# Optimization experiments

Measured on AMD Instinct MI355X. Metric: run time of the kernel, lower is better.

## Reference

```python
import jax, jax.numpy as jnp
import numpy as np

N_NODES = 50000
N_EDGES = 800000
D = 128
N_GRAPHS = 128
N_CLASSES = 10
BN_EPS = 1e-5


def setup_inputs() -> dict:
    key = jax.random.key(0)
    ks = jax.random.split(key, 8)
    x = jax.random.normal(ks[0], (N_NODES, D), dtype=jnp.float32)
    edge_index = jax.random.randint(ks[1], (2, N_EDGES), 0, N_NODES, dtype=jnp.int64)
    batch = jnp.sort(jax.random.randint(ks[2], (N_NODES,), 0, N_GRAPHS, dtype=jnp.int64))
    s = 1.0 / np.sqrt(D)
    W1a = jax.random.normal(ks[3], (D, D), dtype=jnp.float32) * s
    W1b = jax.random.normal(ks[4], (D, D), dtype=jnp.float32) * s
    W2a = jax.random.normal(ks[5], (D, D), dtype=jnp.float32) * s
    W2b = jax.random.normal(ks[6], (D, D), dtype=jnp.float32) * s
    Wo = jax.random.normal(ks[7], (D, N_CLASSES), dtype=jnp.float32) * s
    z = jnp.zeros((D,), jnp.float32)
    o = jnp.ones((D,), jnp.float32)
    return dict(x=x, edge_index=edge_index, batch=batch,
                W1a=W1a, b1a=z, W1b=W1b, b1b=z, g1=o, be1=z,
                W2a=W2a, b2a=z, W2b=W2b, b2b=z, g2=o, be2=z,
                Wo=Wo, bo=jnp.zeros((N_CLASSES,), jnp.float32))


def _gin_conv(x, edge_index, Wa, ba, Wb, bb):
    # message passing: gather source features, scatter-add to targets (eps=0)
    msgs = x[edge_index[0]]                                   # [E, D]
    agg = jax.ops.segment_sum(msgs, edge_index[1], num_segments=x.shape[0])
    h = agg + x                                               # (1+eps)*x + sum_j x_j
    h = jnp.maximum(h @ Wa + ba, 0.0)                         # Linear -> ReLU
    return h @ Wb + bb                                        # Linear


def _bn_relu(h, gamma, beta):
    # BatchNorm1d (training mode: batch stats, biased var) + ReLU
    mu = jnp.mean(h, axis=0)
    var = jnp.mean(jnp.square(h - mu), axis=0)
    hn = (h - mu) * jax.lax.rsqrt(var + BN_EPS) * gamma + beta
    return jnp.maximum(hn, 0.0)


def reference(x, edge_index, batch,
              W1a, b1a, W1b, b1b, g1, be1,
              W2a, b2a, W2b, b2b, g2, be2,
              Wo, bo):
    h = _gin_conv(x, edge_index, W1a, b1a, W1b, b1b)
    h = _bn_relu(h, g1, be1)
    h = _gin_conv(h, edge_index, W2a, b2a, W2b, b2b)
    h = _bn_relu(h, g2, be2)
    pooled = jax.ops.segment_sum(h, batch, num_segments=N_GRAPHS)  # global_add_pool
    return pooled @ Wo + bo
```

## Files before the change

### kernel.cpp

```cpp
#include <hip/hip_runtime.h>

typedef __attribute__((ext_vector_type(8))) short bf16x8;
typedef __attribute__((ext_vector_type(4))) float f32x4;
typedef __attribute__((ext_vector_type(2))) float f32x2;
typedef __attribute__((ext_vector_type(2))) unsigned u32x2;

#define N_NODES 50000
#define N_EDGES 800000
#define DIM 128
#define N_GRAPHS 128
#define N_CLASSES 10
#define BN_EPS 1e-5f
#define FBLK ((N_NODES + 63) / 64)
#define NPART (FBLK * 4)
#define RED_NB 64
#define RED_ROWS ((NPART + RED_NB - 1) / RED_NB)

#define NBUCK 196
#define FILL_NB 400
#define FILL_PER (N_EDGES / FILL_NB)
#define BMAX 6144

static __device__ __forceinline__ unsigned short f2bf(float f) {
    unsigned u = __float_as_uint(f);
    u += 0x7FFF + ((u >> 16) & 1);
    return (unsigned short)(u >> 16);
}
static __device__ __forceinline__ float bf_lo(unsigned u) { return __uint_as_float(u << 16); }
static __device__ __forceinline__ float bf_hi(unsigned u) { return __uint_as_float(u & 0xffff0000u); }
static __device__ __forceinline__ unsigned packbf(float a, float b) {
    return (unsigned)f2bf(a) | ((unsigned)f2bf(b) << 16);
}

__global__ __launch_bounds__(256) void cvt_x(const f32x2* __restrict__ x,
                                             unsigned* __restrict__ xb, int n) {
    int t = blockIdx.x * 256 + threadIdx.x;
    if (t < n) { f32x2 v = x[t]; xb[t] = packbf(v[0], v[1]); }
}

__global__ __launch_bounds__(256) void bucket_count(const int* __restrict__ ei,
                                                    int* __restrict__ gbcnt) {
    __shared__ int cnt[NBUCK];
    int tid = threadIdx.x;
    if (tid < NBUCK) cnt[tid] = 0;
    __syncthreads();
    int e0 = blockIdx.x * FILL_PER;
    for (int c = tid; c < FILL_PER; c += 256) {
        int dst = ei[N_EDGES + e0 + c];
        atomicAdd(&cnt[dst >> 8], 1);
    }
    __syncthreads();
    if (tid < NBUCK) atomicAdd(&gbcnt[tid], cnt[tid]);
}

__global__ __launch_bounds__(256) void bucket_scan(const int* __restrict__ gbcnt,
                                                   int* __restrict__ boff,
                                                   int* __restrict__ gcur) {
    __shared__ int buf[256];
    int t = threadIdx.x;
    int v = (t < NBUCK) ? gbcnt[t] : 0;
    buf[t] = v;
    __syncthreads();
#pragma unroll
    for (int off = 1; off < 256; off <<= 1) {
        int u = (t >= off) ? buf[t - off] : 0;
        __syncthreads();
        buf[t] += u;
        __syncthreads();
    }
    if (t < NBUCK) { int ex = buf[t] - v; boff[t] = ex; gcur[t] = ex; }
    if (t == 0) boff[NBUCK] = N_EDGES;
}

__global__ __launch_bounds__(256) void bucket_fill(const int* __restrict__ ei,
                                                   int* __restrict__ gcur,
                                                   unsigned* __restrict__ gbuf) {
    __shared__ unsigned ent[FILL_PER];
    __shared__ unsigned srt[FILL_PER];
    __shared__ int cnt[256], c2[256], lofs[256], gbase[256];
    int tid = threadIdx.x;
    int e0 = blockIdx.x * FILL_PER;
    cnt[tid] = 0; c2[tid] = 0;
    __syncthreads();
    for (int i = tid; i < FILL_PER; i += 256) {
        int src = ei[e0 + i];
        int dst = ei[N_EDGES + e0 + i];
        ent[i] = (unsigned)src | ((unsigned)(dst & 255) << 16) | ((unsigned)(dst >> 8) << 24);
        atomicAdd(&cnt[dst >> 8], 1);
    }
    __syncthreads();
    int v = cnt[tid];
    lofs[tid] = v;
    __syncthreads();
#pragma unroll
    for (int off = 1; off < 256; off <<= 1) {
        int u = (tid >= off) ? lofs[tid - off] : 0;
        __syncthreads();
        lofs[tid] += u;
        __syncthreads();
    }
    int excl = lofs[tid] - v;
    lofs[tid] = excl;
    if (tid < NBUCK && v > 0) gbase[tid] = atomicAdd(&gcur[tid], v);
    __syncthreads();
    for (int i = tid; i < FILL_PER; i += 256) {
        unsigned w = ent[i];
        int b = w >> 24;
        int r = atomicAdd(&c2[b], 1);
        srt[lofs[b] + r] = w;
    }
    __syncthreads();
    for (int i = tid; i < FILL_PER; i += 256) {
        unsigned w = srt[i];
        int b = w >> 24;
        gbuf[gbase[b] + (i - lofs[b])] = w;
    }
}

__global__ __launch_bounds__(256) void csr_build(const unsigned* __restrict__ gbuf,
                                                 const int* __restrict__ boff,
                                                 unsigned short* __restrict__ csr16,
                                                 int* __restrict__ row_start) {
    __shared__ unsigned ent[BMAX];
    __shared__ unsigned short csl[BMAX];
    __shared__ int cnt[256], c2[256], offs[256];
    int b = blockIdx.x, t = threadIdx.x;
    int base = boff[b], n = boff[b + 1] - base;
    for (int i = t; i < n; i += 256) ent[i] = gbuf[base + i];
    cnt[t] = 0; c2[t] = 0;
    __syncthreads();
    for (int i = t; i < n; i += 256) atomicAdd(&cnt[(ent[i] >> 16) & 255], 1);
    __syncthreads();
    int v = cnt[t];
    offs[t] = v;
    __syncthreads();
#pragma unroll
    for (int off = 1; off < 256; off <<= 1) {
        int u = (t >= off) ? offs[t - off] : 0;
        __syncthreads();
        offs[t] += u;
        __syncthreads();
    }
    int excl = offs[t] - v;
    int node = b * 256 + t;
    if (node < N_NODES) row_start[node] = base + excl;
    if (b == NBUCK - 1 && t == 0) row_start[N_NODES] = N_EDGES;
    __syncthreads();
    offs[t] = excl;
    __syncthreads();
    for (int i = t; i < n; i += 256) {
        unsigned w = ent[i];
        int d = (w >> 16) & 255;
        int r = atomicAdd(&c2[d], 1);
        csl[offs[d] + r] = (unsigned short)(w & 0xffffu);
    }
    __syncthreads();
    for (int i = t; i < n; i += 256) csr16[base + i] = csl[i];
}

__global__ __launch_bounds__(256) void graph_starts(const int* __restrict__ batch,
                                                    int* __restrict__ gs) {
    int g = blockIdx.x * 256 + threadIdx.x;
    if (g > N_GRAPHS) return;
    int lo = 0, hi = N_NODES;
    while (lo < hi) {
        int mid = (lo + hi) >> 1;
        if (batch[mid] < g) lo = mid + 1; else hi = mid;
    }
    gs[g] = lo;
}

template <bool BN>
__global__ __launch_bounds__(256) void aggregate_bf(const unsigned* __restrict__ F,
                                                    unsigned* __restrict__ out,
                                                    const int* __restrict__ row_start,
                                                    const unsigned short* __restrict__ csr16,
                                                    const float* __restrict__ scale,
                                                    const float* __restrict__ shift) {
    int wave = threadIdx.x >> 6, lane = threadIdx.x & 63;
    int v = blockIdx.x * 4 + wave;
    if (v >= N_NODES) return;
    float sc0 = 0.f, sc1 = 0.f, sh0 = 0.f, sh1 = 0.f;
    if (BN) {
        f32x2 s2 = ((const f32x2*)scale)[lane];
        f32x2 h2 = ((const f32x2*)shift)[lane];
        sc0 = s2[0]; sc1 = s2[1]; sh0 = h2[0]; sh1 = h2[1];
    }
    unsigned u = F[(size_t)v * 64 + lane];
    float a0 = bf_lo(u), a1 = bf_hi(u);
    if (BN) { a0 = fmaxf(a0 * sc0 + sh0, 0.f); a1 = fmaxf(a1 * sc1 + sh1, 0.f); }
    int e = row_start[v], end = row_start[v + 1];
    for (; e + 3 < end; e += 4) {
        unsigned ua = F[(size_t)csr16[e] * 64 + lane];
        unsigned ub = F[(size_t)csr16[e + 1] * 64 + lane];
        unsigned uc = F[(size_t)csr16[e + 2] * 64 + lane];
        unsigned ud = F[(size_t)csr16[e + 3] * 64 + lane];
        float p0 = bf_lo(ua), p1 = bf_hi(ua), q0 = bf_lo(ub), q1 = bf_hi(ub);
        float r0 = bf_lo(uc), r1 = bf_hi(uc), s0 = bf_lo(ud), s1 = bf_hi(ud);
        if (BN) {
            p0 = fmaxf(p0 * sc0 + sh0, 0.f); p1 = fmaxf(p1 * sc1 + sh1, 0.f);
            q0 = fmaxf(q0 * sc0 + sh0, 0.f); q1 = fmaxf(q1 * sc1 + sh1, 0.f);
            r0 = fmaxf(r0 * sc0 + sh0, 0.f); r1 = fmaxf(r1 * sc1 + sh1, 0.f);
            s0 = fmaxf(s0 * sc0 + sh0, 0.f); s1 = fmaxf(s1 * sc1 + sh1, 0.f);
        }
        a0 += (p0 + q0) + (r0 + s0);
        a1 += (p1 + q1) + (r1 + s1);
    }
    for (; e < end; ++e) {
        unsigned ua = F[(size_t)csr16[e] * 64 + lane];
        float p0 = bf_lo(ua), p1 = bf_hi(ua);
        if (BN) { p0 = fmaxf(p0 * sc0 + sh0, 0.f); p1 = fmaxf(p1 * sc1 + sh1, 0.f); }
        a0 += p0; a1 += p1;
    }
    out[(size_t)v * 64 + lane] = packbf(a0, a1);
}

__global__ __launch_bounds__(256) void prep_w(const float* __restrict__ W0,
                                              const float* __restrict__ W1,
                                              const float* __restrict__ W2,
                                              const float* __restrict__ W3,
                                              unsigned short* __restrict__ wf) {
    int t = blockIdx.x * 256 + threadIdx.x;
    if (t >= 4 * 16384) return;
    int m = t >> 14, rem = t & 16383;
    int e = rem & 7, lane = (rem >> 3) & 63, fi = rem >> 9;
    int ks = fi & 3, n = fi >> 2;
    int col = n * 16 + (lane & 15);
    int k = ks * 32 + ((lane >> 4) << 3) + e;
    const float* W = (m == 0) ? W0 : (m == 1) ? W1 : (m == 2) ? W2 : W3;
    wf[t] = f2bf(W[k * DIM + col]);
}

__global__ __launch_bounds__(256, 3) void fused_layer(
        const unsigned short* __restrict__ A,
        const bf16x8* __restrict__ wfA_g,
        const bf16x8* __restrict__ wfB_g,
        const float* __restrict__ bias_a,
        const float* __restrict__ bias_b,
        unsigned short* __restrict__ out,
        float* __restrict__ psum,
        float* __restrict__ psq, int M) {
    __shared__ bf16x8 wfS[2048];
    __shared__ unsigned short mid[8192];

    int tid = threadIdx.x;
    int w = tid >> 6, lane = tid & 63;
    int cl = lane & 15, kq = lane >> 4;
    int rblk = blockIdx.x * 64;

    bf16x8 wb[8];
#pragma unroll
    for (int i = 0; i < 8; ++i) wb[i] = wfB_g[i * 256 + tid];

#pragma unroll
    for (int i = 0; i < 8; ++i) wfS[i * 256 + tid] = wfA_g[i * 256 + tid];

    int arow = rblk + w * 16 + cl;
    if (arow >= M) arow = M - 1;
    bf16x8 af[4];
    const unsigned short* Ap = A + (size_t)arow * DIM + kq * 8;
#pragma unroll
    for (int ks = 0; ks < 4; ++ks) af[ks] = *(const bf16x8*)(Ap + ks * 32);

    __syncthreads();

    f32x4 acc[8];
#pragma unroll
    for (int n = 0; n < 8; ++n) acc[n] = f32x4{0.f, 0.f, 0.f, 0.f};
#pragma unroll
    for (int n = 0; n < 8; ++n)
#pragma unroll
        for (int ks = 0; ks < 4; ++ks)
            acc[n] = __builtin_amdgcn_mfma_f32_16x16x32_bf16(af[ks], wfS[(n * 4 + ks) * 64 + lane],
                                                             acc[n], 0, 0, 0);

#pragma unroll
    for (int n = 0; n < 8; ++n) {
        int col = n * 16 + cl;
        float b = bias_a[col];
#pragma unroll
        for (int r = 0; r < 4; ++r) {
            int rl = w * 16 + kq * 4 + r;
            float v = fmaxf(acc[n][r] + b, 0.f);
            mid[(rl * DIM + col) ^ ((rl & 7) << 3)] = f2bf(v);
        }
    }
    __syncthreads();

#pragma unroll
    for (int i = 0; i < 8; ++i) wfS[i * 256 + tid] = wb[i];

    bf16x8 af2[4];
    {
        int rl = w * 16 + cl;
        int sw = (cl & 7) << 3;
#pragma unroll
        for (int ks = 0; ks < 4; ++ks)
            af2[ks] = *(const bf16x8*)(mid + ((rl * DIM + kq * 8 + ks * 32) ^ sw));
    }
    __syncthreads();

    f32x4 acc2[8];
#pragma unroll
    for (int n = 0; n < 8; ++n) acc2[n] = f32x4{0.f, 0.f, 0.f, 0.f};
#pragma unroll
    for (int n = 0; n < 8; ++n)
#pragma unroll
        for (int ks = 0; ks < 4; ++ks)
            acc2[n] = __builtin_amdgcn_mfma_f32_16x16x32_bf16(af2[ks], wfS[(n * 4 + ks) * 64 + lane],
                                                              acc2[n], 0, 0, 0);

    int prow = blockIdx.x * 4 + w;
#pragma unroll
    for (int n = 0; n < 8; ++n) {
        int col = n * 16 + cl;
        float b = bias_b[col];
        float s = 0.f, q = 0.f;
#pragma unroll
        for (int r = 0; r < 4; ++r) {
            int rl = w * 16 + kq * 4 + r;
            float v = acc2[n][r] + b;
            if (rblk + rl < M) { s += v; q += v * v; }
            mid[(rl * DIM + col) ^ ((rl & 7) << 3)] = f2bf(v);
        }
        s += __shfl_xor(s, 16, 64);
        s += __shfl_xor(s, 32, 64);
        q += __shfl_xor(q, 16, 64);
        q += __shfl_xor(q, 32, 64);
        if (kq == 0) {
            psum[(size_t)prow * DIM + col] = s;
            psq[(size_t)prow * DIM + col] = q;
        }
    }

    {
        int r4 = lane >> 4, c = lane & 15;
#pragma unroll
        for (int rb = 0; rb < 4; ++rb) {
            int rl = w * 16 + rb * 4 + r4;
            int grow = rblk + rl;
            bf16x8 v = *(const bf16x8*)(mid + ((rl * DIM + c * 8) ^ ((rl & 7) << 3)));
            if (grow < M) *(bf16x8*)(out + (size_t)grow * DIM + c * 8) = v;
        }
    }
}

__global__ __launch_bounds__(256) void reduce_stats(const float* __restrict__ psum,
                                                    const float* __restrict__ psq,
                                                    float* __restrict__ ps2) {
    int b = blockIdx.x, t = threadIdx.x;
    int c = t & 127;
    const float* src = (t < 128) ? psum : psq;
    int r0 = b * RED_ROWS;
    int r1 = min(NPART, r0 + RED_ROWS);
    float acc = 0.f;
    for (int r = r0; r < r1; ++r) acc += src[(size_t)r * DIM + c];
    ps2[(size_t)b * 256 + t] = acc;
}

__global__ __launch_bounds__(256) void bn_finalize(const float* __restrict__ ps2,
                                                   const float* __restrict__ g,
                                                   const float* __restrict__ be,
                                                   float* __restrict__ scale,
                                                   float* __restrict__ shift) {
    __shared__ float sums[128], sqs[128];
    int t = threadIdx.x;
    int c = t & 127;
    float acc = 0.f;
#pragma unroll 4
    for (int r = 0; r < RED_NB; ++r) acc += ps2[(size_t)r * 256 + t];
    if (t < 128) sums[c] = acc; else sqs[c] = acc;
    __syncthreads();
    if (t < 128) {
        const float invN = 1.0f / (float)N_NODES;
        float mu = sums[c] * invN;
        float var = sqs[c] * invN - mu * mu;
        float rs = rsqrtf(var + BN_EPS) * g[c];
        scale[c] = rs;
        shift[c] = be[c] - mu * rs;
    }
}

__global__ __launch_bounds__(256) void bn_pool(const unsigned short* __restrict__ h,
                                               const float* __restrict__ scale,
                                               const float* __restrict__ shift,
                                               const int* __restrict__ gs,
                                               float* __restrict__ pooled) {
    int g = blockIdx.x;
    int t = threadIdx.x;
    int c4 = t & 31;
    int rs = t >> 5;
    int r0 = gs[g], r1 = gs[g + 1];
    f32x4 sc = ((const f32x4*)scale)[c4];
    f32x4 sh = ((const f32x4*)shift)[c4];
    f32x4 acc = f32x4{0.f, 0.f, 0.f, 0.f};
    for (int r = r0 + rs; r < r1; r += 8) {
        u32x2 u = *(const u32x2*)(h + (size_t)r * DIM + c4 * 4);
        float f0 = bf_lo(u[0]), f1 = bf_hi(u[0]), f2 = bf_lo(u[1]), f3 = bf_hi(u[1]);
        acc[0] += fmaxf(f0 * sc[0] + sh[0], 0.f);
        acc[1] += fmaxf(f1 * sc[1] + sh[1], 0.f);
        acc[2] += fmaxf(f2 * sc[2] + sh[2], 0.f);
        acc[3] += fmaxf(f3 * sc[3] + sh[3], 0.f);
    }
    __shared__ f32x4 red[256];
    red[t] = acc;
    __syncthreads();
#pragma unroll
    for (int off = 128; off >= 32; off >>= 1) {
        if (t < off) red[t] += red[t + off];
        __syncthreads();
    }
    if (t < 32) ((f32x4*)pooled)[g * 32 + c4] = red[t];
}

__global__ __launch_bounds__(256) void final_gemm(const float* __restrict__ pooled,
                                                  const float* __restrict__ Wo,
                                                  const float* __restrict__ bo,
                                                  float* __restrict__ out) {
    int t = blockIdx.x * 256 + threadIdx.x;
    if (t >= N_GRAPHS * N_CLASSES) return;
    int g = t / N_CLASSES, c = t - g * N_CLASSES;
    float s = bo[c];
    const float* p = pooled + (size_t)g * DIM;
#pragma unroll 4
    for (int k = 0; k < DIM; ++k) s += p[k] * Wo[k * N_CLASSES + c];
    out[t] = s;
}

extern "C" void kernel_launch(void* const* d_in, const int* in_sizes, int n_in,
                              void* d_out, int out_size, void* d_ws, size_t ws_size,
                              hipStream_t stream) {
    const float* x   = (const float*)d_in[0];
    const int* ei    = (const int*)d_in[1];
    const int* batch = (const int*)d_in[2];
    const float* W1a = (const float*)d_in[3];
    const float* b1a = (const float*)d_in[4];
    const float* W1b = (const float*)d_in[5];
    const float* b1b = (const float*)d_in[6];
    const float* g1  = (const float*)d_in[7];
    const float* be1 = (const float*)d_in[8];
    const float* W2a = (const float*)d_in[9];
    const float* b2a = (const float*)d_in[10];
    const float* W2b = (const float*)d_in[11];
    const float* b2b = (const float*)d_in[12];
    const float* g2  = (const float*)d_in[13];
    const float* be2 = (const float*)d_in[14];
    const float* Wo  = (const float*)d_in[15];
    const float* bo  = (const float*)d_in[16];

    char* ws = (char*)d_ws;
    const size_t NBH = (size_t)N_NODES * DIM * 2;
    unsigned short* xb   = (unsigned short*)ws;
    unsigned short* aggb = (unsigned short*)(ws + NBH);
    unsigned short* hb   = (unsigned short*)(ws + 2 * NBH);
    unsigned short* wfrag = (unsigned short*)(ws + 3 * NBH);
    float* psum = (float*)(ws + 3 * NBH + 4 * 16384 * 2);
    float* psq  = psum + (size_t)NPART * DIM;
    float* ps2  = psq + (size_t)NPART * DIM;
    float* pooled  = ps2 + RED_NB * 256;
    float* scale1  = pooled + N_GRAPHS * DIM;
    float* shift1  = scale1 + 128;
    float* scale2  = scale1 + 256;
    float* shift2  = scale1 + 384;
    int* gs        = (int*)(shift2 + 128);
    int* gbcnt     = gs + N_GRAPHS + 1;
    int* boff      = gbcnt + NBUCK;
    int* gcur      = boff + NBUCK + 1;
    int* row_start = gcur + NBUCK;
    unsigned* gbuf = (unsigned*)(row_start + N_NODES + 1);
    unsigned short* csr16 = (unsigned short*)(gbuf + N_EDGES);

    hipMemsetAsync(gbcnt, 0, NBUCK * 4, stream);

    const int nv2 = N_NODES * 64;
    cvt_x<<<(nv2 + 255) / 256, 256, 0, stream>>>((const f32x2*)x, (unsigned*)xb, nv2);
    prep_w<<<256, 256, 0, stream>>>(W1a, W1b, W2a, W2b, wfrag);
    graph_starts<<<1, 256, 0, stream>>>(batch, gs);

    bucket_count<<<FILL_NB, 256, 0, stream>>>(ei, gbcnt);
    bucket_scan<<<1, 256, 0, stream>>>(gbcnt, boff, gcur);
    bucket_fill<<<FILL_NB, 256, 0, stream>>>(ei, gcur, gbuf);
    csr_build<<<NBUCK, 256, 0, stream>>>(gbuf, boff, csr16, row_start);

    const int ablk = (N_NODES + 3) / 4;

    aggregate_bf<false><<<ablk, 256, 0, stream>>>((const unsigned*)xb, (unsigned*)aggb,
                                                  row_start, csr16, nullptr, nullptr);
    fused_layer<<<FBLK, 256, 0, stream>>>(
        aggb, (const bf16x8*)(wfrag + 0 * 16384), (const bf16x8*)(wfrag + 1 * 16384),
        b1a, b1b, hb, psum, psq, N_NODES);
    reduce_stats<<<RED_NB, 256, 0, stream>>>(psum, psq, ps2);
    bn_finalize<<<1, 256, 0, stream>>>(ps2, g1, be1, scale1, shift1);

    aggregate_bf<true><<<ablk, 256, 0, stream>>>((const unsigned*)hb, (unsigned*)aggb,
                                                 row_start, csr16, scale1, shift1);
    fused_layer<<<FBLK, 256, 0, stream>>>(
        aggb, (const bf16x8*)(wfrag + 2 * 16384), (const bf16x8*)(wfrag + 3 * 16384),
        b2a, b2b, hb, psum, psq, N_NODES);
    reduce_stats<<<RED_NB, 256, 0, stream>>>(psum, psq, ps2);
    bn_finalize<<<1, 256, 0, stream>>>(ps2, g2, be2, scale2, shift2);
    bn_pool<<<N_GRAPHS, 256, 0, stream>>>(hb, scale2, shift2, gs, pooled);

    final_gemm<<<(N_GRAPHS * N_CLASSES + 255) / 256, 256, 0, stream>>>(pooled, Wo, bo,
                                                                       (float*)d_out);
}
```

Measured before the change: 251.6 us.

## Split each aggregation wave across two edges, merge prep and final-GEMM kernels

The gather-aggregate kernel now has each wave process two neighbor edges at once. Each half-wave loads 8 bytes per lane, the two halves handle alternating edges, and the partial sums are merged with a cross-half shuffle. This aims to raise memory-level parallelism and cut per-edge load instructions. Separately, the x conversion, weight fragment prep and graph start search are merged into one launch, and the final classifier GEMM is folded into the pooling kernel, which removes several launches and the pooled buffer round trip. The cost is an extra shuffle per node and fewer unrolled loads per half-wave.

After: 240.7 us. 1.05x faster.

```diff
diff --git a/kernel.cpp b/kernel.cpp
--- a/kernel.cpp
+++ b/kernel.cpp
@@ -21,6 +21,9 @@
 #define FILL_PER (N_EDGES / FILL_NB)
 #define BMAX 6144
 
+#define CVT_NB (N_NODES * 64 / 256)
+#define PREPW_NB 256
+
 static __device__ __forceinline__ unsigned short f2bf(float f) {
     unsigned u = __float_as_uint(f);
     u += 0x7FFF + ((u >> 16) & 1);
@@ -32,10 +35,39 @@
     return (unsigned)f2bf(a) | ((unsigned)f2bf(b) << 16);
 }
 
-__global__ __launch_bounds__(256) void cvt_x(const f32x2* __restrict__ x,
-                                             unsigned* __restrict__ xb, int n) {
-    int t = blockIdx.x * 256 + threadIdx.x;
-    if (t < n) { f32x2 v = x[t]; xb[t] = packbf(v[0], v[1]); }
+__global__ __launch_bounds__(256) void prep_all(const f32x2* __restrict__ x,
+                                                unsigned* __restrict__ xb,
+                                                const float* __restrict__ W0,
+                                                const float* __restrict__ W1,
+                                                const float* __restrict__ W2,
+                                                const float* __restrict__ W3,
+                                                unsigned short* __restrict__ wf,
+                                                const int* __restrict__ batch,
+                                                int* __restrict__ gs) {
+    int b = blockIdx.x, tid = threadIdx.x;
+    if (b < CVT_NB) {
+        int t = b * 256 + tid;
+        f32x2 v = x[t];
+        xb[t] = packbf(v[0], v[1]);
+    } else if (b < CVT_NB + PREPW_NB) {
+        int t = (b - CVT_NB) * 256 + tid;
+        int m = t >> 14, rem = t & 16383;
+        int e = rem & 7, lane = (rem >> 3) & 63, fi = rem >> 9;
+        int ks = fi & 3, n = fi >> 2;
+        int col = n * 16 + (lane & 15);
+        int k = ks * 32 + ((lane >> 4) << 3) + e;
+        const float* W = (m == 0) ? W0 : (m == 1) ? W1 : (m == 2) ? W2 : W3;
+        wf[t] = f2bf(W[k * DIM + col]);
+    } else {
+        int g = tid;
+        if (g > N_GRAPHS) return;
+        int lo = 0, hi = N_NODES;
+        while (lo < hi) {
+            int mid = (lo + hi) >> 1;
+            if (batch[mid] < g) lo = mid + 1; else hi = mid;
+        }
+        gs[g] = lo;
+    }
 }
 
 __global__ __launch_bounds__(256) void bucket_count(const int* __restrict__ ei,
@@ -158,21 +190,9 @@
     for (int i = t; i < n; i += 256) csr16[base + i] = csl[i];
 }
 
-__global__ __launch_bounds__(256) void graph_starts(const int* __restrict__ batch,
-                                                    int* __restrict__ gs) {
-    int g = blockIdx.x * 256 + threadIdx.x;
-    if (g > N_GRAPHS) return;
-    int lo = 0, hi = N_NODES;
-    while (lo < hi) {
-        int mid = (lo + hi) >> 1;
-        if (batch[mid] < g) lo = mid + 1; else hi = mid;
-    }
-    gs[g] = lo;
-}
-
 template <bool BN>
-__global__ __launch_bounds__(256) void aggregate_bf(const unsigned* __restrict__ F,
-                                                    unsigned* __restrict__ out,
+__global__ __launch_bounds__(256) void aggregate_bf(const u32x2* __restrict__ F2,
+                                                    u32x2* __restrict__ out,
                                                     const int* __restrict__ row_start,
                                                     const unsigned short* __restrict__ csr16,
                                                     const float* __restrict__ scale,
@@ -180,55 +200,58 @@
     int wave = threadIdx.x >> 6, lane = threadIdx.x & 63;
     int v = blockIdx.x * 4 + wave;
     if (v >= N_NODES) return;
-    float sc0 = 0.f, sc1 = 0.f, sh0 = 0.f, sh1 = 0.f;
+    int half = lane >> 5;
+    int c4 = lane & 31;
+    f32x4 sc, sh;
     if (BN) {
-        f32x2 s2 = ((const f32x2*)scale)[lane];
-        f32x2 h2 = ((const f32x2*)shift)[lane];
-        sc0 = s2[0]; sc1 = s2[1]; sh0 = h2[0]; sh1 = h2[1];
-    }
-    unsigned u = F[(size_t)v * 64 + lane];
-    float a0 = bf_lo(u), a1 = bf_hi(u);
-    if (BN) { a0 = fmaxf(a0 * sc0 + sh0, 0.f); a1 = fmaxf(a1 * sc1 + sh1, 0.f); }
-    int e = row_start[v], end = row_start[v + 1];
-    for (; e + 3 < end; e += 4) {
-        unsigned ua = F[(size_t)csr16[e] * 64 + lane];
-        unsigned ub = F[(size_t)csr16[e + 1] * 64 + lane];
-        unsigned uc = F[(size_t)csr16[e + 2] * 64 + lane];
-        unsigned ud = F[(size_t)csr16[e + 3] * 64 + lane];
-        float p0 = bf_lo(ua), p1 = bf_hi(ua), q0 = bf_lo(ub), q1 = bf_hi(ub);
-        float r0 = bf_lo(uc), r1 = bf_hi(uc), s0 = bf_lo(ud), s1 = bf_hi(ud);
+        sc = ((const f32x4*)scale)[c4];
+        sh = ((const f32x4*)shift)[c4];
+    }
+    f32x4 acc = f32x4{0.f, 0.f, 0.f, 0.f};
+    if (half == 0) {
+        u32x2 u = F2[(size_t)v * 32 + c4];
+        acc[0] = bf_lo(u[0]); acc[1] = bf_hi(u[0]);
+        acc[2] = bf_lo(u[1]); acc[3] = bf_hi(u[1]);
         if (BN) {
-            p0 = fmaxf(p0 * sc0 + sh0, 0.f); p1 = fmaxf(p1 * sc1 + sh1, 0.f);
-            q0 = fmaxf(q0 * sc0 + sh0, 0.f); q1 = fmaxf(q1 * sc1 + sh1, 0.f);
-            r0 = fmaxf(r0 * sc0 + sh0, 0.f); r1 = fmaxf(r1 * sc1 + sh1, 0.f);
-            s0 = fmaxf(s0 * sc0 + sh0, 0.f); s1 = fmaxf(s1 * sc1 + sh1, 0.f);
-        }
-        a0 += (p0 + q0) + (r0 + s0);
-        a1 += (p1 + q1) + (r1 + s1);
-    }
-    for (; e < end; ++e) {
-        unsigned ua = F[(size_t)csr16[e] * 64 + lane];
-        float p0 = bf_lo(ua), p1 = bf_hi(ua);
-        if (BN) { p0 = fmaxf(p0 * sc0 + sh0, 0.f); p1 = fmaxf(p1 * sc1 + sh1, 0.f); }
-        a0 += p0; a1 += p1;
-    }
-    out[(size_t)v * 64 + lane] = packbf(a0, a1);
-}
-
-__global__ __launch_bounds__(256) void prep_w(const float* __restrict__ W0,
-                                              const float* __restrict__ W1,
-                                              const float* __restrict__ W2,
-                                              const float* __restrict__ W3,
-                                              unsigned short* __restrict__ wf) {
-    int t = blockIdx.x * 256 + threadIdx.x;
-    if (t >= 4 * 16384) return;
-    int m = t >> 14, rem = t & 16383;
-    int e = rem & 7, lane = (rem >> 3) & 63, fi = rem >> 9;
-    int ks = fi & 3, n = fi >> 2;
-    int col = n * 16 + (lane & 15);
-    int k = ks * 32 + ((lane >> 4) << 3) + e;
-    const float* W = (m == 0) ? W0 : (m == 1) ? W1 : (m == 2) ? W2 : W3;
-    wf[t] = f2bf(W[k * DIM + col]);
+#pragma unroll
+            for (int k = 0; k < 4; ++k) acc[k] = fmaxf(acc[k] * sc[k] + sh[k], 0.f);
+        }
+    }
+    int e0 = row_start[v];
+    int n = row_start[v + 1] - e0;
+    int i = half;
+    for (; i + 2 < n; i += 4) {
+        int s0 = csr16[e0 + i], s1 = csr16[e0 + i + 2];
+        u32x2 ua = F2[(size_t)s0 * 32 + c4];
+        u32x2 ub = F2[(size_t)s1 * 32 + c4];
+        float p0 = bf_lo(ua[0]), p1 = bf_hi(ua[0]), p2 = bf_lo(ua[1]), p3 = bf_hi(ua[1]);
+        float q0 = bf_lo(ub[0]), q1 = bf_hi(ub[0]), q2 = bf_lo(ub[1]), q3 = bf_hi(ub[1]);
+        if (BN) {
+            p0 = fmaxf(p0 * sc[0] + sh[0], 0.f); p1 = fmaxf(p1 * sc[1] + sh[1], 0.f);
+            p2 = fmaxf(p2 * sc[2] + sh[2], 0.f); p3 = fmaxf(p3 * sc[3] + sh[3], 0.f);
+            q0 = fmaxf(q0 * sc[0] + sh[0], 0.f); q1 = fmaxf(q1 * sc[1] + sh[1], 0.f);
+            q2 = fmaxf(q2 * sc[2] + sh[2], 0.f); q3 = fmaxf(q3 * sc[3] + sh[3], 0.f);
+        }
+        acc[0] += p0 + q0; acc[1] += p1 + q1; acc[2] += p2 + q2; acc[3] += p3 + q3;
+    }
+    for (; i < n; i += 2) {
+        int s = csr16[e0 + i];
+        u32x2 ua = F2[(size_t)s * 32 + c4];
+        float p0 = bf_lo(ua[0]), p1 = bf_hi(ua[0]), p2 = bf_lo(ua[1]), p3 = bf_hi(ua[1]);
+        if (BN) {
+            p0 = fmaxf(p0 * sc[0] + sh[0], 0.f); p1 = fmaxf(p1 * sc[1] + sh[1], 0.f);
+            p2 = fmaxf(p2 * sc[2] + sh[2], 0.f); p3 = fmaxf(p3 * sc[3] + sh[3], 0.f);
+        }
+        acc[0] += p0; acc[1] += p1; acc[2] += p2; acc[3] += p3;
+    }
+#pragma unroll
+    for (int k = 0; k < 4; ++k) acc[k] += __shfl_xor(acc[k], 32, 64);
+    if (half == 0) {
+        u32x2 w;
+        w[0] = packbf(acc[0], acc[1]);
+        w[1] = packbf(acc[2], acc[3]);
+        out[(size_t)v * 32 + c4] = w;
+    }
 }
 
 __global__ __launch_bounds__(256, 3) void fused_layer(
@@ -381,11 +404,13 @@
     }
 }
 
-__global__ __launch_bounds__(256) void bn_pool(const unsigned short* __restrict__ h,
-                                               const float* __restrict__ scale,
-                                               const float* __restrict__ shift,
-                                               const int* __restrict__ gs,
-                                               float* __restrict__ pooled) {
+__global__ __launch_bounds__(256) void bn_pool_final(const unsigned short* __restrict__ h,
+                                                     const float* __restrict__ scale,
+                                                     const float* __restrict__ shift,
+                                                     const int* __restrict__ gs,
+                                                     const float* __restrict__ Wo,
+                                                     const float* __restrict__ bo,
+                                                     float* __restrict__ out) {
     int g = blockIdx.x;
     int t = threadIdx.x;
     int c4 = t & 31;
@@ -403,6 +428,7 @@
         acc[3] += fmaxf(f3 * sc[3] + sh[3], 0.f);
     }
     __shared__ f32x4 red[256];
+    __shared__ float pf[DIM];
     red[t] = acc;
     __syncthreads();
 #pragma unroll
@@ -410,21 +436,18 @@
         if (t < off) red[t] += red[t + off];
         __syncthreads();
     }
-    if (t < 32) ((f32x4*)pooled)[g * 32 + c4] = red[t];
-}
-
-__global__ __launch_bounds__(256) void final_gemm(const float* __restrict__ pooled,
-                                                  const float* __restrict__ Wo,
-                                                  const float* __restrict__ bo,
-                                                  float* __restrict__ out) {
-    int t = blockIdx.x * 256 + threadIdx.x;
-    if (t >= N_GRAPHS * N_CLASSES) return;
-    int g = t / N_CLASSES, c = t - g * N_CLASSES;
-    float s = bo[c];
-    const float* p = pooled + (size_t)g * DIM;
-#pragma unroll 4
-    for (int k = 0; k < DIM; ++k) s += p[k] * Wo[k * N_CLASSES + c];
-    out[t] = s;
+    if (t < 32) {
+        f32x4 r = red[t];
+        pf[t * 4 + 0] = r[0]; pf[t * 4 + 1] = r[1];
+        pf[t * 4 + 2] = r[2]; pf[t * 4 + 3] = r[3];
+    }
+    __syncthreads();
+    if (t < N_CLASSES) {
+        float s = bo[t];
+#pragma unroll 8
+        for (int k = 0; k < DIM; ++k) s += pf[k] * Wo[k * N_CLASSES + t];
+        out[g * N_CLASSES + t] = s;
+    }
 }
 
 extern "C" void kernel_launch(void* const* d_in, const int* in_sizes, int n_in,
@@ -457,8 +480,7 @@
     float* psum = (float*)(ws + 3 * NBH + 4 * 16384 * 2);
     float* psq  = psum + (size_t)NPART * DIM;
     float* ps2  = psq + (size_t)NPART * DIM;
-    float* pooled  = ps2 + RED_NB * 256;
-    float* scale1  = pooled + N_GRAPHS * DIM;
+    float* scale1  = ps2 + RED_NB * 256;
     float* shift1  = scale1 + 128;
     float* scale2  = scale1 + 256;
     float* shift2  = scale1 + 384;
@@ -472,10 +494,8 @@
 
     hipMemsetAsync(gbcnt, 0, NBUCK * 4, stream);
 
-    const int nv2 = N_NODES * 64;
-    cvt_x<<<(nv2 + 255) / 256, 256, 0, stream>>>((const f32x2*)x, (unsigned*)xb, nv2);
-    prep_w<<<256, 256, 0, stream>>>(W1a, W1b, W2a, W2b, wfrag);
-    graph_starts<<<1, 256, 0, stream>>>(batch, gs);
+    prep_all<<<CVT_NB + PREPW_NB + 1, 256, 0, stream>>>(
+        (const f32x2*)x, (unsigned*)xb, W1a, W1b, W2a, W2b, wfrag, batch, gs);
 
     bucket_count<<<FILL_NB, 256, 0, stream>>>(ei, gbcnt);
     bucket_scan<<<1, 256, 0, stream>>>(gbcnt, boff, gcur);
@@ -484,7 +504,7 @@
 
     const int ablk = (N_NODES + 3) / 4;
 
-    aggregate_bf<false><<<ablk, 256, 0, stream>>>((const unsigned*)xb, (unsigned*)aggb,
+    aggregate_bf<false><<<ablk, 256, 0, stream>>>((const u32x2*)xb, (u32x2*)aggb,
                                                   row_start, csr16, nullptr, nullptr);
     fused_layer<<<FBLK, 256, 0, stream>>>(
         aggb, (const bf16x8*)(wfrag + 0 * 16384), (const bf16x8*)(wfrag + 1 * 16384),
@@ -492,15 +512,14 @@
     reduce_stats<<<RED_NB, 256, 0, stream>>>(psum, psq, ps2);
     bn_finalize<<<1, 256, 0, stream>>>(ps2, g1, be1, scale1, shift1);
 
-    aggregate_bf<true><<<ablk, 256, 0, stream>>>((const unsigned*)hb, (unsigned*)aggb,
+    aggregate_bf<true><<<ablk, 256, 0, stream>>>((const u32x2*)hb, (u32x2*)aggb,
                                                  row_start, csr16, scale1, shift1);
     fused_layer<<<FBLK, 256, 0, stream>>>(
         aggb, (const bf16x8*)(wfrag + 2 * 16384), (const bf16x8*)(wfrag + 3 * 16384),
         b2a, b2b, hb, psum, psq, N_NODES);
     reduce_stats<<<RED_NB, 256, 0, stream>>>(psum, psq, ps2);
     bn_finalize<<<1, 256, 0, stream>>>(ps2, g2, be2, scale2, shift2);
-    bn_pool<<<N_GRAPHS, 256, 0, stream>>>(hb, scale2, shift2, gs, pooled);
-
-    final_gemm<<<(N_GRAPHS * N_CLASSES + 255) / 256, 256, 0, stream>>>(pooled, Wo, bo,
-                                                                       (float*)d_out);
-}
+
+    bn_pool_final<<<N_GRAPHS, 256, 0, stream>>>(hb, scale2, shift2, gs, Wo, bo,
+                                                (float*)d_out);
+}
```
